# Kernel tuning notes

Hardware: AMD Instinct MI355X
Metric: run time of the kernel (lower is better)

## Reference

```python
import jax, jax.numpy as jnp
import numpy as np

GAMMA = 1.0
INPUT_DIM = 512
NUM_CENTERS = 4096
BATCH = 16384


def setup_inputs() -> dict:
    key = jax.random.key(0)
    kx, kc = jax.random.split(key)
    x = jax.random.normal(kx, (BATCH, INPUT_DIM), dtype=jnp.float32)
    centers = jax.random.normal(kc, (NUM_CENTERS, INPUT_DIM), dtype=jnp.float32)
    return {"x": x, "centers": centers}


def reference(x, centers):
    x_sq = jnp.sum(x * x, axis=-1, keepdims=True)            # [B, 1]
    c_sq = jnp.sum(centers * centers, axis=-1)               # [C]
    cross = jnp.einsum("bd,cd->bc", x, centers)              # [B, C]
    dist_sq = x_sq - 2.0 * cross + c_sq[None, :]
    return jnp.exp(-GAMMA * dist_sq)
```

## Files before the change

### kernel.cpp

```cpp
#include <hip/hip_runtime.h>
#include <stdint.h>

#define M_DIM 16384
#define N_DIM 4096
#define K_DIM 512
#define TPB 8

typedef int v8i __attribute__((ext_vector_type(8)));
typedef float f32x16 __attribute__((ext_vector_type(16)));
typedef float f32x4v __attribute__((ext_vector_type(4)));

typedef __attribute__((address_space(3))) uint32_t lds_u32_t;
typedef const __attribute__((address_space(1))) uint32_t glob_u32_t;

__device__ __forceinline__ void gload16(const void* g, void* l) {
    __builtin_amdgcn_global_load_lds((glob_u32_t*)g, (lds_u32_t*)l, 16, 0, 0);
}

__global__ __launch_bounds__(256)
void convert_norm_kernel(const float* __restrict__ X, const float* __restrict__ C,
                         uint8_t* __restrict__ Apack, uint8_t* __restrict__ Bf8,
                         float* __restrict__ xsq, float* __restrict__ csq) {
    const int wave = threadIdx.x >> 6;
    const int lane = threadIdx.x & 63;
    const int row = blockIdx.x * 4 + wave;

    const float* src;
    uint8_t* dst;
    float* nrm;
    int r;
    size_t off;
    if (row < M_DIM) {
        src = X; dst = Apack; nrm = xsq; r = row;
        off = (size_t)((r >> 5) * 8 + (lane >> 3)) * 2048
            + ((lane >> 2) & 1) * 1024 + (r & 31) * 32 + (lane & 3) * 8;
    } else {
        src = C; dst = Bf8; nrm = csq; r = row - M_DIM;
        off = (size_t)r * K_DIM + lane * 8;
    }

    const float4* p = (const float4*)(src + (size_t)r * K_DIM) + lane * 2;
    float4 a = p[0], b = p[1];
    uint32_t lo = 0, hi = 0;
    lo = __builtin_amdgcn_cvt_pk_fp8_f32(a.x, a.y, lo, false);
    lo = __builtin_amdgcn_cvt_pk_fp8_f32(a.z, a.w, lo, true);
    hi = __builtin_amdgcn_cvt_pk_fp8_f32(b.x, b.y, hi, false);
    hi = __builtin_amdgcn_cvt_pk_fp8_f32(b.z, b.w, hi, true);
    *(uint2*)(dst + off) = make_uint2(lo, hi);

    float s = a.x*a.x + a.y*a.y + a.z*a.z + a.w*a.w
            + b.x*b.x + b.y*b.y + b.z*b.z + b.w*b.w;
    #pragma unroll
    for (int o2 = 32; o2 > 0; o2 >>= 1) s += __shfl_down(s, o2, 64);
    if (lane == 0) nrm[r] = s;
}

__global__ __launch_bounds__(256, 2)
void rbf_mfma_kernel(const uint8_t* __restrict__ Apack, const uint8_t* __restrict__ B8,
                     const float* __restrict__ xsq, const float* __restrict__ csq,
                     float* __restrict__ out) {
    __shared__ uint8_t Bs[128 * 512];

    const int tid = threadIdx.x;
    const int lv  = tid & 63;
    const int w   = tid >> 6;
    const int h   = lv >> 5;
    const int r31 = lv & 31;

    const int bs = blockIdx.x & 31;
    const int mg = blockIdx.x >> 5;
    const int bn = bs * 128;

    {
        const int seg = (lv >> 3) & 3;
        const int tc  = lv & 7;
        const int pb  = 2 * w + h;
        const int cc  = (tc - pb) & 7;
        const int gcb = seg * 8 + cc;
        #pragma unroll
        for (int R = 0; R < 16; ++R) {
            const int p = 8 * R + pb;
            const int col = bn + 4 * (p & 31) + (p >> 5);
            gload16(B8 + (size_t)col * K_DIM + gcb * 16,
                    Bs + R * 4096 + w * 1024 + lv * 16);
        }
    }
    __syncthreads();

    const float4 cs4 = *(const float4*)(csq + bn + 4 * r31);

    for (int t = 0; t < TPB; ++t) {
        const int bm = (mg * TPB + t) * 128;
        const uint8_t* aB = Apack + (size_t)((bm >> 5) + w) * 16384
                          + h * 1024 + r31 * 32;

        f32x16 acc[4] = {};

        #pragma unroll
        for (int ks = 0; ks < 8; ++ks) {
            uint4 a0 = *(const uint4*)(aB + ks * 2048);
            uint4 a1 = *(const uint4*)(aB + ks * 2048 + 16);
            v8i av = (v8i){(int)a0.x, (int)a0.y, (int)a0.z, (int)a0.w,
                           (int)a1.x, (int)a1.y, (int)a1.z, (int)a1.w};
            const uint8_t* segp = Bs + (ks >> 1) * 128;
            const int cw = (ks & 1) * 4 + 2 * h;
            const int s0 = ((cw + 0 + r31) & 7) * 16;
            const int s1 = ((cw + 1 + r31) & 7) * 16;
            #pragma unroll
            for (int j = 0; j < 4; ++j) {
                const uint8_t* rowp = segp + (size_t)(j * 32 + r31) * 512;
                uint4 lo = *(const uint4*)(rowp + s0);
                uint4 hi = *(const uint4*)(rowp + s1);
                v8i bv = (v8i){(int)lo.x, (int)lo.y, (int)lo.z, (int)lo.w,
                               (int)hi.x, (int)hi.y, (int)hi.z, (int)hi.w};
                acc[j] = __builtin_amdgcn_mfma_scale_f32_32x32x64_f8f6f4(
                    av, bv, acc[j],
                    0 , 0 ,
                    0, 0x7F7F7F7Fu, 0, 0x7F7F7F7Fu);
            }
        }

        const int mbase = bm + 32 * w + 4 * h;
        #pragma unroll
        for (int g = 0; g < 4; ++g) {
            const float4 xs4 = *(const float4*)(xsq + mbase + 8 * g);
            #pragma unroll
            for (int rr = 0; rr < 4; ++rr) {
                const int reg = g * 4 + rr;
                const float xs = (rr == 0) ? xs4.x : (rr == 1) ? xs4.y
                               : (rr == 2) ? xs4.z : xs4.w;
                const int gm = mbase + 8 * g + rr;
                f32x4v o;
                o.x = __expf(-(xs - 2.0f * acc[0][reg] + cs4.x));
                o.y = __expf(-(xs - 2.0f * acc[1][reg] + cs4.y));
                o.z = __expf(-(xs - 2.0f * acc[2][reg] + cs4.z));
                o.w = __expf(-(xs - 2.0f * acc[3][reg] + cs4.w));
                __builtin_nontemporal_store(
                    o, (f32x4v*)(out + (size_t)gm * N_DIM + bn + 4 * r31));
            }
        }
    }
}

extern "C" void kernel_launch(void* const* d_in, const int* in_sizes, int n_in,
                              void* d_out, int out_size, void* d_ws, size_t ws_size,
                              hipStream_t stream) {
    const float* X = (const float*)d_in[0];
    const float* C = (const float*)d_in[1];
    float* out = (float*)d_out;

    uint8_t* Apack = (uint8_t*)d_ws;
    uint8_t* Bf8 = Apack + (size_t)M_DIM * K_DIM;
    float* xsq = (float*)(Bf8 + (size_t)N_DIM * K_DIM);
    float* csq = xsq + M_DIM;

    convert_norm_kernel<<<(M_DIM + N_DIM) / 4, 256, 0, stream>>>(X, C, Apack, Bf8, xsq, csq);
    rbf_mfma_kernel<<<32 * (M_DIM / 128 / TPB), 256, 0, stream>>>(Apack, Bf8, xsq, csq, out);
}
```

Before: 352.6 us.

## Stream B tile through small LDS K-chunks, one output tile per block

Before, each block staged a 128x512 FP8 B tile in 64KB of LDS and reused it across 8 M-tiles. Now each block computes a single 128x128 output tile and loads B in four 128-byte K-chunks into a 16KB LDS buffer, with barriers between chunks. Launch bounds rise to 4 blocks per CU and the grid grows eightfold. The goal is higher occupancy so the exp/store-bound epilogue of some blocks overlaps with the loads and MFMA of others, at the cost of losing B reuse across M-tiles and adding per-chunk synchronisation without double buffering.

```diff
diff --git a/kernel.cpp b/kernel.cpp
--- a/kernel.cpp
+++ b/kernel.cpp
@@ -4,7 +4,6 @@
 #define M_DIM 16384
 #define N_DIM 4096
 #define K_DIM 512
-#define TPB 8
 
 typedef int v8i __attribute__((ext_vector_type(8)));
 typedef float f32x16 __attribute__((ext_vector_type(16)));
@@ -55,11 +54,11 @@
     if (lane == 0) nrm[r] = s;
 }
 
-__global__ __launch_bounds__(256, 2)
+__global__ __launch_bounds__(256, 4)
 void rbf_mfma_kernel(const uint8_t* __restrict__ Apack, const uint8_t* __restrict__ B8,
                      const float* __restrict__ xsq, const float* __restrict__ csq,
                      float* __restrict__ out) {
-    __shared__ uint8_t Bs[128 * 512];
+    __shared__ uint8_t Bs[128 * 128];
 
     const int tid = threadIdx.x;
     const int lv  = tid & 63;
@@ -67,50 +66,47 @@
     const int h   = lv >> 5;
     const int r31 = lv & 31;
 
-    const int bs = blockIdx.x & 31;
-    const int mg = blockIdx.x >> 5;
-    const int bn = bs * 128;
+    const int bn = (blockIdx.x & 31) * 128;
+    const int bm = (blockIdx.x >> 5) * 128;
 
-    {
-        const int seg = (lv >> 3) & 3;
-        const int tc  = lv & 7;
-        const int pb  = 2 * w + h;
-        const int cc  = (tc - pb) & 7;
-        const int gcb = seg * 8 + cc;
+    const int tr = tid >> 3;
+    const int tc = tid & 7;
+    const int cc = (tc - tr) & 7;
+    const uint8_t* gB = B8 + (size_t)(bn + 4 * tr) * K_DIM + cc * 16;
+    uint8_t* BsW = Bs + w * 1024;
+
+    const uint8_t* aB = Apack + (size_t)((bm >> 5) + w) * 16384 + h * 1024 + r31 * 32;
+
+    const uint8_t* bRow = Bs + r31 * 128;
+
+    f32x16 acc[4] = {};
+
+    for (int kk = 0; kk < 4; ++kk) {
+        const int koff = kk * 128;
         #pragma unroll
-        for (int R = 0; R < 16; ++R) {
-            const int p = 8 * R + pb;
-            const int col = bn + 4 * (p & 31) + (p >> 5);
-            gload16(B8 + (size_t)col * K_DIM + gcb * 16,
-                    Bs + R * 4096 + w * 1024 + lv * 16);
+        for (int R = 0; R < 4; ++R)
+            gload16(gB + koff + (size_t)R * K_DIM, BsW + R * 4096);
+
+        uint4 a0[2], a1[2];
+        #pragma unroll
+        for (int ksl = 0; ksl < 2; ++ksl) {
+            const uint8_t* ap = aB + (2 * kk + ksl) * 2048;
+            a0[ksl] = *(const uint4*)(ap);
+            a1[ksl] = *(const uint4*)(ap + 16);
         }
-    }
-    __syncthreads();
-
-    const float4 cs4 = *(const float4*)(csq + bn + 4 * r31);
-
-    for (int t = 0; t < TPB; ++t) {
-        const int bm = (mg * TPB + t) * 128;
-        const uint8_t* aB = Apack + (size_t)((bm >> 5) + w) * 16384
-                          + h * 1024 + r31 * 32;
-
-        f32x16 acc[4] = {};
+        __syncthreads();
 
         #pragma unroll
-        for (int ks = 0; ks < 8; ++ks) {
-            uint4 a0 = *(const uint4*)(aB + ks * 2048);
-            uint4 a1 = *(const uint4*)(aB + ks * 2048 + 16);
-            v8i av = (v8i){(int)a0.x, (int)a0.y, (int)a0.z, (int)a0.w,
-                           (int)a1.x, (int)a1.y, (int)a1.z, (int)a1.w};
-            const uint8_t* segp = Bs + (ks >> 1) * 128;
-            const int cw = (ks & 1) * 4 + 2 * h;
-            const int s0 = ((cw + 0 + r31) & 7) * 16;
-            const int s1 = ((cw + 1 + r31) & 7) * 16;
+        for (int ksl = 0; ksl < 2; ++ksl) {
+            v8i av = (v8i){(int)a0[ksl].x, (int)a0[ksl].y, (int)a0[ksl].z, (int)a0[ksl].w,
+                           (int)a1[ksl].x, (int)a1[ksl].y, (int)a1[ksl].z, (int)a1[ksl].w};
+            const int c0 = ksl * 4 + 2 * h;
+            const int s0 = ((c0 + 0 + r31) & 7) * 16;
+            const int s1 = ((c0 + 1 + r31) & 7) * 16;
             #pragma unroll
             for (int j = 0; j < 4; ++j) {
-                const uint8_t* rowp = segp + (size_t)(j * 32 + r31) * 512;
-                uint4 lo = *(const uint4*)(rowp + s0);
-                uint4 hi = *(const uint4*)(rowp + s1);
+                uint4 lo = *(const uint4*)(bRow + j * 4096 + s0);
+                uint4 hi = *(const uint4*)(bRow + j * 4096 + s1);
                 v8i bv = (v8i){(int)lo.x, (int)lo.y, (int)lo.z, (int)lo.w,
                                (int)hi.x, (int)hi.y, (int)hi.z, (int)hi.w};
                 acc[j] = __builtin_amdgcn_mfma_scale_f32_32x32x64_f8f6f4(
@@ -119,25 +115,28 @@
                     0, 0x7F7F7F7Fu, 0, 0x7F7F7F7Fu);
             }
         }
+        if (kk < 3) __syncthreads();
+    }
 
-        const int mbase = bm + 32 * w + 4 * h;
+    const float4 cs4 = *(const float4*)(csq + bn + 4 * r31);
+    const int mbase = bm + 32 * w + 4 * h;
+
+    #pragma unroll
+    for (int g = 0; g < 4; ++g) {
+        const float4 xs4 = *(const float4*)(xsq + mbase + 8 * g);
         #pragma unroll
-        for (int g = 0; g < 4; ++g) {
-            const float4 xs4 = *(const float4*)(xsq + mbase + 8 * g);
-            #pragma unroll
-            for (int rr = 0; rr < 4; ++rr) {
-                const int reg = g * 4 + rr;
-                const float xs = (rr == 0) ? xs4.x : (rr == 1) ? xs4.y
-                               : (rr == 2) ? xs4.z : xs4.w;
-                const int gm = mbase + 8 * g + rr;
-                f32x4v o;
-                o.x = __expf(-(xs - 2.0f * acc[0][reg] + cs4.x));
-                o.y = __expf(-(xs - 2.0f * acc[1][reg] + cs4.y));
-                o.z = __expf(-(xs - 2.0f * acc[2][reg] + cs4.z));
-                o.w = __expf(-(xs - 2.0f * acc[3][reg] + cs4.w));
-                __builtin_nontemporal_store(
-                    o, (f32x4v*)(out + (size_t)gm * N_DIM + bn + 4 * r31));
-            }
+        for (int rr = 0; rr < 4; ++rr) {
+            const int reg = g * 4 + rr;
+            const float xs = (rr == 0) ? xs4.x : (rr == 1) ? xs4.y
+                           : (rr == 2) ? xs4.z : xs4.w;
+            const int gm = mbase + 8 * g + rr;
+            f32x4v o;
+            o.x = __expf(-(xs - 2.0f * acc[0][reg] + cs4.x));
+            o.y = __expf(-(xs - 2.0f * acc[1][reg] + cs4.y));
+            o.z = __expf(-(xs - 2.0f * acc[2][reg] + cs4.z));
+            o.w = __expf(-(xs - 2.0f * acc[3][reg] + cs4.w));
+            __builtin_nontemporal_store(
+                o, (f32x4v*)(out + (size_t)gm * N_DIM + bn + 4 * r31));
         }
     }
 }
@@ -155,5 +154,5 @@
     float* csq = xsq + M_DIM;
 
     convert_norm_kernel<<<(M_DIM + N_DIM) / 4, 256, 0, stream>>>(X, C, Apack, Bf8, xsq, csq);
-    rbf_mfma_kernel<<<32 * (M_DIM / 128 / TPB), 256, 0, stream>>>(Apack, Bf8, xsq, csq, out);
+    rbf_mfma_kernel<<<(M_DIM / 128) * (N_DIM / 128), 256, 0, stream>>>(Apack, Bf8, xsq, csq, out);
 }
```

Result: faster. 301.1 us, median of 2 (-14.6%).

## Halve N tile to 64 columns and raise occupancy to four blocks per CU

Applied to the files above, without the earlier changes.

Shrinks each block's tile of centers from 128 to 64 columns, so the LDS tile is halved and the accumulators drop from four 32x32 MFMA tiles to two. Row tiles per block go from 8 to 4, and the grid is rebuilt over 64-column strips, giving 4x as many blocks. Launch bounds now ask for 4 blocks per CU and the LDS swizzle is redone for a full 512-byte row. The goal is more waves to hide memory latency while output is written. The cost is that A-operand fragments are reused across fewer columns, so global A traffic doubles, and stores shrink from 16-byte to 8-byte vectors.

```diff
diff --git a/kernel.cpp b/kernel.cpp
--- a/kernel.cpp
+++ b/kernel.cpp
@@ -4,11 +4,11 @@
 #define M_DIM 16384
 #define N_DIM 4096
 #define K_DIM 512
-#define TPB 8
+#define TPB 4
 
 typedef int v8i __attribute__((ext_vector_type(8)));
 typedef float f32x16 __attribute__((ext_vector_type(16)));
-typedef float f32x4v __attribute__((ext_vector_type(4)));
+typedef float f32x2v __attribute__((ext_vector_type(2)));
 
 typedef __attribute__((address_space(3))) uint32_t lds_u32_t;
 typedef const __attribute__((address_space(1))) uint32_t glob_u32_t;
@@ -55,11 +55,11 @@
     if (lane == 0) nrm[r] = s;
 }
 
-__global__ __launch_bounds__(256, 2)
+__global__ __launch_bounds__(256, 4)
 void rbf_mfma_kernel(const uint8_t* __restrict__ Apack, const uint8_t* __restrict__ B8,
                      const float* __restrict__ xsq, const float* __restrict__ csq,
                      float* __restrict__ out) {
-    __shared__ uint8_t Bs[128 * 512];
+    __shared__ uint8_t Bs[64 * 512];
 
     const int tid = threadIdx.x;
     const int lv  = tid & 63;
@@ -67,34 +67,33 @@
     const int h   = lv >> 5;
     const int r31 = lv & 31;
 
-    const int bs = blockIdx.x & 31;
-    const int mg = blockIdx.x >> 5;
-    const int bn = bs * 128;
+    const int bn = (blockIdx.x & 63) * 64;
+    const int mg = blockIdx.x >> 6;
 
-    {
-        const int seg = (lv >> 3) & 3;
-        const int tc  = lv & 7;
-        const int pb  = 2 * w + h;
-        const int cc  = (tc - pb) & 7;
-        const int gcb = seg * 8 + cc;
-        #pragma unroll
-        for (int R = 0; R < 16; ++R) {
-            const int p = 8 * R + pb;
-            const int col = bn + 4 * (p & 31) + (p >> 5);
-            gload16(B8 + (size_t)col * K_DIM + gcb * 16,
-                    Bs + R * 4096 + w * 1024 + lv * 16);
-        }
+    #pragma unroll
+    for (int R = 0; R < 8; ++R) {
+        const int p = 8 * R + 2 * w + h;
+        const int c = (r31 - p) & 31;
+        const int col = bn + 2 * (p & 31) + (p >> 5);
+        gload16(B8 + (size_t)col * K_DIM + c * 16,
+                Bs + R * 4096 + w * 1024);
     }
     __syncthreads();
 
-    const float4 cs4 = *(const float4*)(csq + bn + 4 * r31);
+    const float2 cs2 = *(const float2*)(csq + bn + 2 * r31);
 
     for (int t = 0; t < TPB; ++t) {
         const int bm = (mg * TPB + t) * 128;
+        const int mbase = bm + 32 * w + 4 * h;
+
+        float4 xs4[4];
+        #pragma unroll
+        for (int g = 0; g < 4; ++g) xs4[g] = *(const float4*)(xsq + mbase + 8 * g);
+
         const uint8_t* aB = Apack + (size_t)((bm >> 5) + w) * 16384
                           + h * 1024 + r31 * 32;
 
-        f32x16 acc[4] = {};
+        f32x16 acc[2] = {};
 
         #pragma unroll
         for (int ks = 0; ks < 8; ++ks) {
@@ -102,15 +101,14 @@
             uint4 a1 = *(const uint4*)(aB + ks * 2048 + 16);
             v8i av = (v8i){(int)a0.x, (int)a0.y, (int)a0.z, (int)a0.w,
                            (int)a1.x, (int)a1.y, (int)a1.z, (int)a1.w};
-            const uint8_t* segp = Bs + (ks >> 1) * 128;
-            const int cw = (ks & 1) * 4 + 2 * h;
-            const int s0 = ((cw + 0 + r31) & 7) * 16;
-            const int s1 = ((cw + 1 + r31) & 7) * 16;
+            const int c0 = 4 * ks + 2 * h;
+            const int s0 = ((c0 + 0 + r31) & 31) * 16;
+            const int s1 = ((c0 + 1 + r31) & 31) * 16;
             #pragma unroll
-            for (int j = 0; j < 4; ++j) {
-                const uint8_t* rowp = segp + (size_t)(j * 32 + r31) * 512;
-                uint4 lo = *(const uint4*)(rowp + s0);
-                uint4 hi = *(const uint4*)(rowp + s1);
+            for (int j = 0; j < 2; ++j) {
+                const uint8_t* rp = Bs + (size_t)(32 * j + r31) * 512;
+                uint4 lo = *(const uint4*)(rp + s0);
+                uint4 hi = *(const uint4*)(rp + s1);
                 v8i bv = (v8i){(int)lo.x, (int)lo.y, (int)lo.z, (int)lo.w,
                                (int)hi.x, (int)hi.y, (int)hi.z, (int)hi.w};
                 acc[j] = __builtin_amdgcn_mfma_scale_f32_32x32x64_f8f6f4(
@@ -120,23 +118,19 @@
             }
         }
 
-        const int mbase = bm + 32 * w + 4 * h;
         #pragma unroll
         for (int g = 0; g < 4; ++g) {
-            const float4 xs4 = *(const float4*)(xsq + mbase + 8 * g);
             #pragma unroll
             for (int rr = 0; rr < 4; ++rr) {
-                const int reg = g * 4 + rr;
-                const float xs = (rr == 0) ? xs4.x : (rr == 1) ? xs4.y
-                               : (rr == 2) ? xs4.z : xs4.w;
+                const int reg = 4 * g + rr;
+                const float xs = (rr == 0) ? xs4[g].x : (rr == 1) ? xs4[g].y
+                               : (rr == 2) ? xs4[g].z : xs4[g].w;
                 const int gm = mbase + 8 * g + rr;
-                f32x4v o;
-                o.x = __expf(-(xs - 2.0f * acc[0][reg] + cs4.x));
-                o.y = __expf(-(xs - 2.0f * acc[1][reg] + cs4.y));
-                o.z = __expf(-(xs - 2.0f * acc[2][reg] + cs4.z));
-                o.w = __expf(-(xs - 2.0f * acc[3][reg] + cs4.w));
+                f32x2v o;
+                o.x = __expf(-(xs - 2.0f * acc[0][reg] + cs2.x));
+                o.y = __expf(-(xs - 2.0f * acc[1][reg] + cs2.y));
                 __builtin_nontemporal_store(
-                    o, (f32x4v*)(out + (size_t)gm * N_DIM + bn + 4 * r31));
+                    o, (f32x2v*)(out + (size_t)gm * N_DIM + bn + 2 * r31));
             }
         }
     }
@@ -155,5 +149,5 @@
     float* csq = xsq + M_DIM;
 
     convert_norm_kernel<<<(M_DIM + N_DIM) / 4, 256, 0, stream>>>(X, C, Apack, Bf8, xsq, csq);
-    rbf_mfma_kernel<<<32 * (M_DIM / 128 / TPB), 256, 0, stream>>>(Apack, Bf8, xsq, csq, out);
+    rbf_mfma_kernel<<<(N_DIM / 64) * (M_DIM / 128 / TPB), 256, 0, stream>>>(Apack, Bf8, xsq, csq, out);
 }
```

Measured after the change: 523.6 us. 48.5% more time.
